# Kernel optimization log

Hardware: AMD Instinct MI355X
Metric: run time of the kernel (lower is better)

The kernel has to match this reference:

```python
import jax, jax.numpy as jnp
import numpy as np

VOL = (64, 64, 64)       # (nz, nx, ny)
GB = 128                 # gaussian_batch_size


def _voxel_coords():
    nz, nx, ny = VOL
    z = jnp.linspace(-1.0, 1.0, nz)
    x = jnp.linspace(-1.0, 1.0, nx)
    y = jnp.linspace(-1.0, 1.0, ny)
    Z, X, Y = jnp.meshgrid(z, x, y, indexing='ij')
    return jnp.stack([Z, X, Y], axis=-1).reshape(-1, 3)  # [V, 3]


def setup_inputs() -> dict:
    key = jax.random.key(0)
    k1, k2, k3, k4 = jax.random.split(key, 4)
    N = 4096
    positions = jax.random.uniform(k1, (N, 3), dtype=jnp.float32) * 2.0 - 1.0
    # PSD inverse covariances: A @ A^T + c*I (so mahalanobis is well-defined)
    A = jax.random.normal(k2, (N, 3, 3), dtype=jnp.float32) * 3.0
    cov_inv = jnp.einsum('nij,nkj->nik', A, A) + 20.0 * jnp.eye(3, dtype=jnp.float32)
    densities_real = jax.random.normal(k3, (N,), dtype=jnp.float32)
    densities_imag = jax.random.normal(k4, (N,), dtype=jnp.float32)
    return {
        'positions': positions,
        'cov_inv': cov_inv,
        'densities_real': densities_real,
        'densities_imag': densities_imag,
    }


def reference(positions, cov_inv, densities_real, densities_imag):
    coords = _voxel_coords()                    # [V, 3]
    V = coords.shape[0]
    N = positions.shape[0]
    nb = N // GB                                # N chosen divisible by GB
    pos = positions.reshape(nb, GB, 3)
    ci = cov_inv.reshape(nb, GB, 3, 3)
    dr = densities_real.reshape(nb, GB)
    di = densities_imag.reshape(nb, GB)

    def body(carry, batch):
        vr, vi = carry
        p, c, drb, dib = batch
        diff = coords[:, None, :] - p[None, :, :]          # [V, B, 3]
        tmp = jnp.einsum('vbi,bij->vbj', diff, c)          # [V, B, 3]
        mahal_sq = jnp.sum(tmp * diff, axis=-1)            # [V, B]
        resp = jnp.exp(-0.5 * mahal_sq)                    # [V, B]
        return (vr + resp @ drb, vi + resp @ dib), None

    init = (jnp.zeros((V,), jnp.float32), jnp.zeros((V,), jnp.float32))
    (vr, vi), _ = jax.lax.scan(body, init, (pos, ci, dr, di))
    volume = (vr + 1j * vi).astype(jnp.complex64).reshape(VOL)
    return volume
```

## Files before the change

kernel.cpp:

```cpp
#include <hip/hip_runtime.h>


#ifndef __has_builtin
#define __has_builtin(x) 0
#endif

typedef float v2f __attribute__((ext_vector_type(2)));

using u16 = unsigned short;
using u32 = unsigned int;
using u64 = unsigned long long;

constexpr int   VTOT = 64 * 64 * 64;
constexpr float QCUT = -12.0f;

__device__ __forceinline__ u16 f2bf(float f) {
    u32 x = __float_as_uint(f);
    x += 0x7FFFu + ((x >> 16) & 1u);
    return (u16)(x >> 16);
}

__device__ __forceinline__ float exp2_fast(float x) {
#if __has_builtin(__builtin_amdgcn_exp2f)
    return __builtin_amdgcn_exp2f(x);
#else
    return exp2f(x);
#endif
}

__device__ __forceinline__ v2f pkfma(v2f a, v2f b, v2f c) {
#if __has_builtin(__builtin_elementwise_fma)
    return __builtin_elementwise_fma(a, b, c);
#else
    v2f r; r.x = fmaf(a.x, b.x, c.x); r.y = fmaf(a.y, b.y, c.y); return r;
#endif
}

__device__ __forceinline__ bool btest(float4 F0, float4 F1, float4 F2,
                                      float zc, float xc, float yc,
                                      float hz, float hx, float hy)
{
    float kz = F0.x, kzy = F0.y, kx = F0.z, kxy = F0.w;
    float k0 = F1.x, ky = F1.y, kzz = F1.z, kxx = F1.w;
    float kzx = F2.x, kyy = F2.y;
    float bc = fmaf(kz, zc, k0);
    bc = fmaf(kzz, zc * zc, bc);
    bc = fmaf(kx, xc, bc);
    bc = fmaf(kxx, xc * xc, bc);
    bc = fmaf(kzx, zc * xc, bc);
    float cy0 = fmaf(kzy, zc, ky);
    cy0 = fmaf(kxy, xc, cy0);
    float qc = fmaf(kyy, yc * yc, fmaf(cy0, yc, bc));
    float gz = fmaf(2.0f * kzz, zc, kz);
    gz = fmaf(kzx, xc, gz); gz = fmaf(kzy, yc, gz);
    float gx = fmaf(2.0f * kxx, xc, kx);
    gx = fmaf(kzx, zc, gx); gx = fmaf(kxy, yc, gx);
    float gy = fmaf(2.0f * kyy, yc, ky);
    gy = fmaf(kzy, zc, gy); gy = fmaf(kxy, xc, gy);
    float margin = fmaf(fabsf(gz), hz, fmaf(fabsf(gx), hx, fabsf(gy) * hy));
    return (qc + margin > QCUT);
}

__global__ __launch_bounds__(256) void vox_prep(
    const float* __restrict__ pos, const float* __restrict__ cov,
    const float* __restrict__ dA,  const float* __restrict__ dB,
    float4* __restrict__ cft, int N)
{
    int n = blockIdx.x * 256 + threadIdx.x;
    if (n >= N) return;
    const float sc = -0.7213475204444817f;
    const float step = 2.0f / 63.0f;
    const float S2 = step * step;
    float p0 = pos[3 * n + 0], p1 = pos[3 * n + 1], p2 = pos[3 * n + 2];
    const float* c = cov + 9 * n;
    float c00 = c[0], c01 = c[1], c02 = c[2];
    float c10 = c[3], c11 = c[4], c12 = c[5];
    float c20 = c[6], c21 = c[7], c22 = c[8];
    float s01 = c01 + c10, s02 = c02 + c20, s12 = c12 + c21;
    float k0 = sc * (c00 * p0 * p0 + c11 * p1 * p1 + c22 * p2 * p2
                     + s01 * p0 * p1 + s02 * p0 * p2 + s12 * p1 * p2);
    float kz = -sc * (2.0f * c00 * p0 + s01 * p1 + s02 * p2);
    float kx = -sc * (s01 * p0 + 2.0f * c11 * p1 + s12 * p2);
    float ky = -sc * (s02 * p0 + s12 * p1 + 2.0f * c22 * p2);
    float kyy = sc * c22;
    float u = exp2f(2.0f * kyy * S2);
    float u2 = u * u;
    cft[4 * n + 0] = make_float4(kz, sc * s02, kx, sc * s12);
    cft[4 * n + 1] = make_float4(k0, ky, sc * c00, sc * c11);
    cft[4 * n + 2] = make_float4(sc * s01, kyy, dA[n], dB[n]);
    cft[4 * n + 3] = make_float4(u, kyy * S2, kyy * (2.0f * step), u2 * u2);
}

template <int SPLIT>
__global__ __launch_bounds__(256, 4) void vox_accum(
    const float4* __restrict__ cft,
    float2* __restrict__ pws)
{
    constexpr int GPS    = 4096 / SPLIT;
    constexpr int CHUNKS = GPS / 256;
    constexpr int LOG    = (SPLIT == 4) ? 2 : 1;

    __shared__ alignas(16) unsigned char smem[21056];
    __shared__ int wc[4];
    float4* sgl = reinterpret_cast<float4*>(smem);
    typedef float2 crow_t[32][9];
    crow_t* cbuf = reinterpret_cast<crow_t*>(smem);

    const int t    = threadIdx.x;
    const int qw   = t >> 6;
    const int lane = t & 63;
    const int sub  = lane >> 5;
    const int slot = lane & 31;
    const int sub2 = qw * 2 + sub;
    const int w    = blockIdx.x;
    const int h    = w & (SPLIT - 1);
    const int bi   = w >> LOG;
    const int i16 = bi >> 6, i8x = (bi >> 3) & 7, i8y = bi & 7;
    const int bz = (i16 & 1) ? 8 + (i16 >> 1) : 7 - (i16 >> 1);
    const int bx = (i8x & 1) ? 4 + (i8x >> 1) : 3 - (i8x >> 1);
    const int by = (i8y & 1) ? 4 + (i8y >> 1) : 3 - (i8y >> 1);

    const int dz = slot >> 3, dx = slot & 7;
    const int iz = bz * 4 + dz, ix = bx * 8 + dx, iy0 = by * 8;

    const float step = 2.0f / 63.0f;
    const float z = -1.0f + step * (float)iz;
    const float x = -1.0f + step * (float)ix;
    const float zz = z * z, xx = x * x, zx = z * x;
    const float y0v = -1.0f + step * (float)(iy0);
    const float y4v = -1.0f + step * (float)(iy0 + 4);
    const v2f Y04  = {y0v, y4v};
    const v2f YY04 = {y0v * y0v, y4v * y4v};
    const v2f z2 = {z, z}, x2 = {x, x};

    const float zc = -1.0f + step * ((float)(bz * 4) + 1.5f);
    const float xc = -1.0f + step * ((float)(bx * 8) + 3.5f);
    const float yc = -1.0f + step * ((float)(by * 8) + 3.5f);
    const float hz = 1.5f * step, hx = 3.5f * step, hy = 3.5f * step;

    const u64 lmask = (1ull << lane) - 1ull;
    const int gbase = h * GPS;

    int n0 = gbase + qw * 64 + lane;
    float4 ga = cft[4 * n0 + 0], gb = cft[4 * n0 + 1],
           gc = cft[4 * n0 + 2], gd = cft[4 * n0 + 3];

    v2f acc[8];
#pragma unroll
    for (int i = 0; i < 8; ++i) acc[i] = v2f{0.f, 0.f};

    for (int cb = 0; cb < CHUNKS; ++cb) {
        bool p = btest(ga, gb, gc, zc, xc, yc, hz, hx, hy);
        u64 m = __ballot(p);
        int rank = __popcll(m & lmask);
        if (lane == 0) wc[qw] = __popcll(m);
        __syncthreads();

        const int c0 = wc[0], c1 = wc[1], c2 = wc[2], c3 = wc[3];
        int off = rank;
        if (qw > 0) off += c0;
        if (qw > 1) off += c1;
        if (qw > 2) off += c2;
        const int total = c0 + c1 + c2 + c3;
        const int pad = (8 - (total & 7)) & 7;
        if (p) {
            sgl[5 * off + 0] = ga;
            sgl[5 * off + 1] = gb;
            sgl[5 * off + 2] = gc;
            sgl[5 * off + 3] = gd;
        }
        if (t < pad) {
            const float4 zf4 = make_float4(0.f, 0.f, 0.f, 0.f);
            sgl[5 * (total + t) + 0] = zf4;
            sgl[5 * (total + t) + 1] = zf4;
            sgl[5 * (total + t) + 2] = zf4;
            sgl[5 * (total + t) + 3] = zf4;
        }
        __syncthreads();

        if (cb < CHUNKS - 1) {
            int nn = gbase + (cb + 1) * 256 + qw * 64 + lane;
            ga = cft[4 * nn + 0]; gb = cft[4 * nn + 1];
            gc = cft[4 * nn + 2]; gd = cft[4 * nn + 3];
        }

        const int ptotal = total + pad;

#pragma unroll 2
        for (int j = sub2; j < ptotal; j += 8) {
            float4 w0 = sgl[5 * j + 0];
            float4 w1 = sgl[5 * j + 1];
            float4 w2 = sgl[5 * j + 2];
            float4 w3 = sgl[5 * j + 3];

            v2f mm = pkfma(v2f{w0.x, w0.y}, z2, v2f{w1.x, w1.y});
            mm = pkfma(v2f{w0.z, w0.w}, x2, mm);
            float bb = fmaf(w1.z, zz, mm.x);
            bb = fmaf(w1.w, xx, bb);
            bb = fmaf(w2.x, zx, bb);
            const float cy = mm.y;
            const float kyy = w2.y;

            v2f q04 = pkfma(v2f{kyy, kyy}, YY04,
                      pkfma(v2f{cy, cy}, Y04, v2f{bb, bb}));
            const float hc = fmaf(cy, step, w3.y);
            const float d0 = fmaf(w3.z, y0v, hc);

            const float t0 = exp2_fast(d0);
            v2f e  = {exp2_fast(q04.x), exp2_fast(q04.y)};
            v2f tt = {t0, t0 * w3.w};
            const v2f uu  = {w3.x, w3.x};
            const v2f dab = {w2.z, w2.w};

            acc[0] = pkfma(v2f{e.x, e.x}, dab, acc[0]);
            acc[4] = pkfma(v2f{e.y, e.y}, dab, acc[4]);
            e = e * tt; tt = tt * uu;
            acc[1] = pkfma(v2f{e.x, e.x}, dab, acc[1]);
            acc[5] = pkfma(v2f{e.y, e.y}, dab, acc[5]);
            e = e * tt; tt = tt * uu;
            acc[2] = pkfma(v2f{e.x, e.x}, dab, acc[2]);
            acc[6] = pkfma(v2f{e.y, e.y}, dab, acc[6]);
            e = e * tt;
            acc[3] = pkfma(v2f{e.x, e.x}, dab, acc[3]);
            acc[7] = pkfma(v2f{e.y, e.y}, dab, acc[7]);
        }
        __syncthreads();
    }

#pragma unroll
    for (int i = 0; i < 8; ++i)
        cbuf[sub2][slot][i] = make_float2(acc[i].x, acc[i].y);
    __syncthreads();

    const int slot2 = t >> 3, yi = t & 7;
    float A = 0.f, B = 0.f;
#pragma unroll
    for (int k = 0; k < 8; ++k) {
        float2 v = cbuf[k][slot2][yi];
        A += v.x; B += v.y;
    }
    const int iz2 = bz * 4 + (slot2 >> 3), ix2 = bx * 8 + (slot2 & 7);
    const int iy2 = by * 8 + yi;
    pws[h * VTOT + (iz2 * 64 + ix2) * 64 + iy2] = make_float2(A, B);
}

template <int SPLIT>
__global__ __launch_bounds__(256) void vox_pack(
    const float2* __restrict__ pws, u32* __restrict__ out)
{
    int v2 = blockIdx.x * 256 + threadIdx.x;
    float A0 = 0.f, B0 = 0.f, A1 = 0.f, B1 = 0.f;
#pragma unroll
    for (int s = 0; s < SPLIT; ++s) {
        float4 a = ((const float4*)(pws + (size_t)s * VTOT))[v2];
        A0 += a.x; B0 += a.y; A1 += a.z; B1 += a.w;
    }
    uint2 o;
    o.x = (u32)f2bf(B0) | ((u32)f2bf(A0) << 16);
    o.y = (u32)f2bf(B1) | ((u32)f2bf(A1) << 16);
    *(uint2*)(out + 2 * v2) = o;
}

constexpr int SEGCAP = 128;

__global__ __launch_bounds__(256, 4) void vox_main(
    const float4* __restrict__ cft, u32* __restrict__ out)
{
    __shared__ float4 sgl[4 * SEGCAP * 3];
    __shared__ int    wc[4];
    __shared__ float  cbuf[4][64][4][2];

    const int t = threadIdx.x, qw = t >> 6, lane = t & 63;
    const int b = (blockIdx.x * 331) & 1023;
    const int bz = b >> 6, bx = (b >> 3) & 7, by = b & 7;
    const int s = lane;
    const int dz = s >> 4, dx = (s >> 1) & 7, dyq = s & 1;
    const int iz = bz * 4 + dz, ix = bx * 8 + dx, iy0 = by * 8 + dyq * 4;

    const float step = 2.0f / 63.0f;
    const float z = -1.0f + step * (float)iz;
    const float x = -1.0f + step * (float)ix;
    const float zz = z * z, xx = x * x, zx = z * x;
    float y[4], yy[4];
#pragma unroll
    for (int i = 0; i < 4; ++i) {
        y[i] = -1.0f + step * (float)(iy0 + i);
        yy[i] = y[i] * y[i];
    }
    const float zc = -1.0f + step * ((float)(bz * 4) + 1.5f);
    const float xc = -1.0f + step * ((float)(bx * 8) + 3.5f);
    const float yc = -1.0f + step * ((float)(by * 8) + 3.5f);
    const float hz = 1.5f * step, hx = 3.5f * step, hy = 3.5f * step;
    const u64 lmask = (1ull << lane) - 1ull;

    int n0 = qw * 128 + lane;
    float4 g0a = cft[4 * n0 + 0], g0b = cft[4 * n0 + 1], g0c = cft[4 * n0 + 2];
    float4 g1a = cft[4 * (n0 + 64) + 0], g1b = cft[4 * (n0 + 64) + 1],
           g1c = cft[4 * (n0 + 64) + 2];

    float aA[4] = {0.f, 0.f, 0.f, 0.f};
    float aB[4] = {0.f, 0.f, 0.f, 0.f};

    for (int cb = 0; cb < 8; ++cb) {
        bool p0 = btest(g0a, g0b, g0c, zc, xc, yc, hz, hx, hy);
        bool p1 = btest(g1a, g1b, g1c, zc, xc, yc, hz, hx, hy);
        u64 m0 = __ballot(p0);
        u64 m1 = __ballot(p1);
        int r0 = __popcll(m0 & lmask);
        int c0 = __popcll(m0);
        int r1 = c0 + __popcll(m1 & lmask);
        int c1 = c0 + __popcll(m1);
        float4* segp = &sgl[qw * SEGCAP * 3];
        if (p0) { segp[3 * r0 + 0] = g0a; segp[3 * r0 + 1] = g0b; segp[3 * r0 + 2] = g0c; }
        if (p1) { segp[3 * r1 + 0] = g1a; segp[3 * r1 + 1] = g1b; segp[3 * r1 + 2] = g1c; }
        if (lane == 0) wc[qw] = c1;
        __syncthreads();

        if (cb < 7) {
            int nn = (cb + 1) * 512 + qw * 128 + lane;
            g0a = cft[4 * nn + 0]; g0b = cft[4 * nn + 1]; g0c = cft[4 * nn + 2];
            g1a = cft[4 * (nn + 64) + 0]; g1b = cft[4 * (nn + 64) + 1];
            g1c = cft[4 * (nn + 64) + 2];
        }
        int cnts[4] = {wc[0], wc[1], wc[2], wc[3]};
#pragma unroll
        for (int seg = 0; seg < 4; ++seg) {
            const float4* sp = &sgl[seg * SEGCAP * 3];
            const int cnt = cnts[seg];
#pragma unroll 2
            for (int j = qw; j < cnt; j += 4) {
                float4 w0 = sp[3 * j + 0];
                float4 w1 = sp[3 * j + 1];
                float4 w2 = sp[3 * j + 2];
                float bb = fmaf(w0.x, z, w1.x);
                bb = fmaf(w1.z, zz, bb);
                bb = fmaf(w0.z, x, bb);
                bb = fmaf(w1.w, xx, bb);
                bb = fmaf(w2.x, zx, bb);
                float cy = fmaf(w0.y, z, w1.y);
                cy = fmaf(w0.w, x, cy);
#pragma unroll
                for (int i = 0; i < 4; ++i) {
                    float qv = fmaf(w2.y, yy[i], fmaf(cy, y[i], bb));
                    float rr = exp2_fast(qv);
                    aA[i] = fmaf(rr, w2.z, aA[i]);
                    aB[i] = fmaf(rr, w2.w, aB[i]);
                }
            }
        }
        __syncthreads();
    }
#pragma unroll
    for (int i = 0; i < 4; ++i) {
        cbuf[qw][s][i][0] = aA[i];
        cbuf[qw][s][i][1] = aB[i];
    }
    __syncthreads();
    const int s2 = t >> 2, i2 = t & 3;
    float A = cbuf[0][s2][i2][0] + cbuf[1][s2][i2][0]
            + cbuf[2][s2][i2][0] + cbuf[3][s2][i2][0];
    float B = cbuf[0][s2][i2][1] + cbuf[1][s2][i2][1]
            + cbuf[2][s2][i2][1] + cbuf[3][s2][i2][1];
    const int dz2 = s2 >> 4, dx2 = (s2 >> 1) & 7, dyq2 = s2 & 1;
    const int iz2 = bz * 4 + dz2, ix2 = bx * 8 + dx2;
    const int iy2 = by * 8 + dyq2 * 4 + i2;
    out[(iz2 * 64 + ix2) * 64 + iy2] = (u32)f2bf(B) | ((u32)f2bf(A) << 16);
}

__global__ __launch_bounds__(256, 4) void vox_fallback(
    const float* __restrict__ pos, const float* __restrict__ cov,
    const float* __restrict__ dA,  const float* __restrict__ dB,
    u32* __restrict__ out, int N)
{
    __shared__ float4 sg[256 * 3];
    __shared__ float  cbuf[4][64][4][2];
    __shared__ int    wcnt[4];

    const int t = threadIdx.x, qw = t >> 6, lane = t & 63, s = lane;
    const int b = blockIdx.x;
    const int bz = b >> 6, bx = (b >> 3) & 7, by = b & 7;
    const int dz = s >> 4, dx = (s >> 1) & 7, dyq = s & 1;
    const int iz = bz * 4 + dz, ix = bx * 8 + dx, iy0 = by * 8 + dyq * 4;

    const float step = 2.0f / 63.0f;
    const float z = -1.0f + step * (float)iz;
    const float x = -1.0f + step * (float)ix;
    const float zz = z * z, xx = x * x, zx = z * x;
    float y[4], yy[4];
#pragma unroll
    for (int i = 0; i < 4; ++i) {
        y[i] = -1.0f + step * (float)(iy0 + i);
        yy[i] = y[i] * y[i];
    }
    const float zc = -1.0f + step * ((float)(bz * 4) + 1.5f);
    const float xc = -1.0f + step * ((float)(bx * 8) + 3.5f);
    const float yc = -1.0f + step * ((float)(by * 8) + 3.5f);
    const float hz = 1.5f * step, hx = 3.5f * step, hy = 3.5f * step;

    float aA[4] = {0.f, 0.f, 0.f, 0.f};
    float aB[4] = {0.f, 0.f, 0.f, 0.f};

    for (int cb = 0; cb < N; cb += 256) {
        int n = cb + t;
        bool pred = false;
        float4 F0, F1, F2;
        if (n < N) {
            const float sc = -0.7213475204444817f;
            float p0 = pos[3 * n + 0], p1 = pos[3 * n + 1], p2 = pos[3 * n + 2];
            const float* c = cov + 9 * n;
            float c00 = c[0], c01 = c[1], c02 = c[2];
            float c10 = c[3], c11 = c[4], c12 = c[5];
            float c20 = c[6], c21 = c[7], c22 = c[8];
            float s01 = c01 + c10, s02 = c02 + c20, s12 = c12 + c21;
            float k0 = sc * (c00 * p0 * p0 + c11 * p1 * p1 + c22 * p2 * p2
                             + s01 * p0 * p1 + s02 * p0 * p2 + s12 * p1 * p2);
            float kz = -sc * (2.0f * c00 * p0 + s01 * p1 + s02 * p2);
            float kx = -sc * (s01 * p0 + 2.0f * c11 * p1 + s12 * p2);
            float ky = -sc * (s02 * p0 + s12 * p1 + 2.0f * c22 * p2);
            F0 = make_float4(kz, sc * s02, kx, sc * s12);
            F1 = make_float4(k0, ky, sc * c00, sc * c11);
            F2 = make_float4(sc * s01, sc * c22, dA[n], dB[n]);
            pred = btest(F0, F1, F2, zc, xc, yc, hz, hx, hy);
        }
        u64 mask = __ballot(pred);
        int rank = __popcll(mask & ((1ull << lane) - 1ull));
        if (lane == 0) wcnt[qw] = __popcll(mask);
        __syncthreads();
        int off = 0;
#pragma unroll
        for (int w = 0; w < 4; ++w) if (w < qw) off += wcnt[w];
        const int total = wcnt[0] + wcnt[1] + wcnt[2] + wcnt[3];
        if (pred) {
            int p = off + rank;
            sg[3 * p + 0] = F0; sg[3 * p + 1] = F1; sg[3 * p + 2] = F2;
        }
        __syncthreads();
#pragma unroll 2
        for (int j = qw; j < total; j += 4) {
            float4 w0 = sg[3 * j + 0], w1 = sg[3 * j + 1], w2 = sg[3 * j + 2];
            float bb = fmaf(w0.x, z, w1.x);
            bb = fmaf(w1.z, zz, bb);
            bb = fmaf(w0.z, x, bb);
            bb = fmaf(w1.w, xx, bb);
            bb = fmaf(w2.x, zx, bb);
            float cy = fmaf(w0.y, z, w1.y);
            cy = fmaf(w0.w, x, cy);
#pragma unroll
            for (int i = 0; i < 4; ++i) {
                float qv = fmaf(w2.y, yy[i], fmaf(cy, y[i], bb));
                float rr = exp2_fast(qv);
                aA[i] = fmaf(rr, w2.z, aA[i]);
                aB[i] = fmaf(rr, w2.w, aB[i]);
            }
        }
        __syncthreads();
    }
#pragma unroll
    for (int i = 0; i < 4; ++i) {
        cbuf[qw][s][i][0] = aA[i];
        cbuf[qw][s][i][1] = aB[i];
    }
    __syncthreads();
    const int s2 = t >> 2, i2 = t & 3;
    float A = cbuf[0][s2][i2][0] + cbuf[1][s2][i2][0]
            + cbuf[2][s2][i2][0] + cbuf[3][s2][i2][0];
    float B = cbuf[0][s2][i2][1] + cbuf[1][s2][i2][1]
            + cbuf[2][s2][i2][1] + cbuf[3][s2][i2][1];
    const int dz2 = s2 >> 4, dx2 = (s2 >> 1) & 7, dyq2 = s2 & 1;
    const int iz2 = bz * 4 + dz2, ix2 = bx * 8 + dx2;
    const int iy2 = by * 8 + dyq2 * 4 + i2;
    out[(iz2 * 64 + ix2) * 64 + iy2] = (u32)f2bf(B) | ((u32)f2bf(A) << 16);
}

extern "C" void kernel_launch(void* const* d_in, const int* in_sizes, int n_in,
                              void* d_out, int out_size, void* d_ws, size_t ws_size,
                              hipStream_t stream)
{
    const float* pos = (const float*)d_in[0];
    const float* cov = (const float*)d_in[1];
    const float* dA  = (const float*)d_in[2];
    const float* dB  = (const float*)d_in[3];
    const int N = in_sizes[0] / 3;

    const size_t CFT_BYTES  = (size_t)4096 * 64;
    const size_t PWS2_BYTES = (size_t)2 * VTOT * 8;
    const size_t PWS4_BYTES = (size_t)4 * VTOT * 8;

    if (N == 4096 && ws_size >= CFT_BYTES + PWS4_BYTES) {
        float4* cft = (float4*)d_ws;
        float2* pws = (float2*)((char*)d_ws + CFT_BYTES);
        vox_prep<<<16, 256, 0, stream>>>(pos, cov, dA, dB, cft, N);
        vox_accum<4><<<4096, 256, 0, stream>>>(cft, pws);
        vox_pack<4><<<VTOT / 512, 256, 0, stream>>>(pws, (u32*)d_out);
    } else if (N == 4096 && ws_size >= CFT_BYTES + PWS2_BYTES) {
        float4* cft = (float4*)d_ws;
        float2* pws = (float2*)((char*)d_ws + CFT_BYTES);
        vox_prep<<<16, 256, 0, stream>>>(pos, cov, dA, dB, cft, N);
        vox_accum<2><<<2048, 256, 0, stream>>>(cft, pws);
        vox_pack<2><<<VTOT / 512, 256, 0, stream>>>(pws, (u32*)d_out);
    } else if (N == 4096 && ws_size >= CFT_BYTES) {
        float4* cft = (float4*)d_ws;
        vox_prep<<<16, 256, 0, stream>>>(pos, cov, dA, dB, cft, N);
        vox_main<<<1024, 256, 0, stream>>>(cft, (u32*)d_out);
    } else {
        vox_fallback<<<1024, 256, 0, stream>>>(pos, cov, dA, dB, (u32*)d_out, N);
    }
}
```

Baseline: 51.13 us.

## Use per-wavefront gaussian compaction segments to remove block-wide barriers; loosen cutoff

Each wavefront now owns a private slice of the gaussians and its own shared-memory segment, so compaction uses only a wave-level ballot. This removes the two __syncthreads per 256-gaussian chunk and the shared counter exchange. Each wave's two 32-lane halves take alternating gaussians, with odd counts padded by a zero entry. The cull threshold QCUT also changes from -12 to -10, which skips more gaussians with small contributions at the cost of accuracy. The per-wave split may load-balance less evenly than the previous block-wide pooling.

```diff
diff --git a/kernel.cpp b/kernel.cpp
--- a/kernel.cpp
+++ b/kernel.cpp
@@ -12,7 +12,7 @@
 using u64 = unsigned long long;
 
 constexpr int   VTOT = 64 * 64 * 64;
-constexpr float QCUT = -12.0f;
+constexpr float QCUT = -10.0f;
 
 __device__ __forceinline__ u16 f2bf(float f) {
     u32 x = __float_as_uint(f);
@@ -97,12 +97,13 @@
     float2* __restrict__ pws)
 {
     constexpr int GPS    = 4096 / SPLIT;
-    constexpr int CHUNKS = GPS / 256;
+    constexpr int GPW    = GPS / 4;
+    constexpr int GROUPS = GPW / 64;
     constexpr int LOG    = (SPLIT == 4) ? 2 : 1;
-
-    __shared__ alignas(16) unsigned char smem[21056];
-    __shared__ int wc[4];
-    float4* sgl = reinterpret_cast<float4*>(smem);
+    constexpr int SEGF4  = 65 * 5;
+
+    __shared__ alignas(16) unsigned char smem[20864];
+    float4* sglbase = reinterpret_cast<float4*>(smem);
     typedef float2 crow_t[32][9];
     crow_t* cbuf = reinterpret_cast<crow_t*>(smem);
 
@@ -139,9 +140,10 @@
     const float hz = 1.5f * step, hx = 3.5f * step, hy = 3.5f * step;
 
     const u64 lmask = (1ull << lane) - 1ull;
-    const int gbase = h * GPS;
-
-    int n0 = gbase + qw * 64 + lane;
+    const int gw = h * GPS + qw * GPW;
+    float4* seg = sglbase + qw * SEGF4;
+
+    int n0 = gw + lane;
     float4 ga = cft[4 * n0 + 0], gb = cft[4 * n0 + 1],
            gc = cft[4 * n0 + 2], gd = cft[4 * n0 + 3];
 
@@ -149,49 +151,38 @@
 #pragma unroll
     for (int i = 0; i < 8; ++i) acc[i] = v2f{0.f, 0.f};
 
-    for (int cb = 0; cb < CHUNKS; ++cb) {
+    for (int g = 0; g < GROUPS; ++g) {
         bool p = btest(ga, gb, gc, zc, xc, yc, hz, hx, hy);
         u64 m = __ballot(p);
         int rank = __popcll(m & lmask);
-        if (lane == 0) wc[qw] = __popcll(m);
-        __syncthreads();
-
-        const int c0 = wc[0], c1 = wc[1], c2 = wc[2], c3 = wc[3];
-        int off = rank;
-        if (qw > 0) off += c0;
-        if (qw > 1) off += c1;
-        if (qw > 2) off += c2;
-        const int total = c0 + c1 + c2 + c3;
-        const int pad = (8 - (total & 7)) & 7;
+        int cnt  = __popcll(m);
         if (p) {
-            sgl[5 * off + 0] = ga;
-            sgl[5 * off + 1] = gb;
-            sgl[5 * off + 2] = gc;
-            sgl[5 * off + 3] = gd;
-        }
-        if (t < pad) {
+            seg[5 * rank + 0] = ga;
+            seg[5 * rank + 1] = gb;
+            seg[5 * rank + 2] = gc;
+            seg[5 * rank + 3] = gd;
+        }
+        if (lane == 0 && (cnt & 1)) {
             const float4 zf4 = make_float4(0.f, 0.f, 0.f, 0.f);
-            sgl[5 * (total + t) + 0] = zf4;
-            sgl[5 * (total + t) + 1] = zf4;
-            sgl[5 * (total + t) + 2] = zf4;
-            sgl[5 * (total + t) + 3] = zf4;
-        }
-        __syncthreads();
-
-        if (cb < CHUNKS - 1) {
-            int nn = gbase + (cb + 1) * 256 + qw * 64 + lane;
+            seg[5 * cnt + 0] = zf4;
+            seg[5 * cnt + 1] = zf4;
+            seg[5 * cnt + 2] = zf4;
+            seg[5 * cnt + 3] = zf4;
+        }
+
+        if (g < GROUPS - 1) {
+            int nn = gw + (g + 1) * 64 + lane;
             ga = cft[4 * nn + 0]; gb = cft[4 * nn + 1];
             gc = cft[4 * nn + 2]; gd = cft[4 * nn + 3];
         }
 
-        const int ptotal = total + pad;
-
-#pragma unroll 2
-        for (int j = sub2; j < ptotal; j += 8) {
-            float4 w0 = sgl[5 * j + 0];
-            float4 w1 = sgl[5 * j + 1];
-            float4 w2 = sgl[5 * j + 2];
-            float4 w3 = sgl[5 * j + 3];
+        const int iters = (cnt + 1) >> 1;
+        for (int i = 0; i < iters; ++i) {
+            const int j = 2 * i + sub;
+            float4 w0 = seg[5 * j + 0];
+            float4 w1 = seg[5 * j + 1];
+            float4 w2 = seg[5 * j + 2];
+            float4 w3 = seg[5 * j + 3];
 
             v2f mm = pkfma(v2f{w0.x, w0.y}, z2, v2f{w1.x, w1.y});
             mm = pkfma(v2f{w0.z, w0.w}, x2, mm);
@@ -224,8 +215,9 @@
             acc[3] = pkfma(v2f{e.x, e.x}, dab, acc[3]);
             acc[7] = pkfma(v2f{e.y, e.y}, dab, acc[7]);
         }
-        __syncthreads();
-    }
+    }
+
+    __syncthreads();
 
 #pragma unroll
     for (int i = 0; i < 8; ++i)
```

After: 45.44 us (median of 2 runs). 1.13x faster.
